# Performance work log

Measured on AMD Instinct MI355X. Metric: run time of the kernel, lower is better.

The kernel has to match this reference:

```python
import jax, jax.numpy as jnp
import numpy as np

T = 0.07          # temperature (params[1])
B, N, D, C = 128, 100000, 128, 40  # batch, bank size (outputSize=K), feat dim (inputSize-1), n classes
STDV = 1.0 / np.sqrt((D + 1) / 3.0)  # init scale from __init__


def setup_inputs() -> dict:
    key = jax.random.key(0)
    k1, k2, k3, k4, k5, k6 = jax.random.split(key, 6)
    x = jax.random.normal(k1, (B, D), dtype=jnp.float32)
    x = x / jnp.linalg.norm(x, axis=1, keepdims=True)  # unit-norm features (keeps exp(out/T) in range)
    y = jax.random.randint(k2, (B,), 0, N)
    labels = jax.random.randint(k3, (B,), 0, C)
    bank_labels = jax.random.randint(k4, (N,), 0, C).astype(jnp.float32)
    mem_feats = (jax.random.uniform(k5, (N, D), dtype=jnp.float32) * 2.0 - 1.0) * STDV
    da_feats = (jax.random.uniform(k6, (N, D), dtype=jnp.float32) * 2.0 - 1.0) * STDV
    memory = jnp.concatenate([bank_labels[:, None], mem_feats], axis=1)      # [N, 1+D], col 0 = label
    memory_da = jnp.concatenate([bank_labels[:, None], da_feats], axis=1)    # [N, 1+D], col 0 = label
    return {"x": x, "y": y, "labels": labels, "memory_da": memory_da, "memory": memory}


def reference(x, y, labels, memory_da, memory):
    # NCEFunction.forward: out[b,n] = exp(x[b] . memory_da[n,1:] / T), Z-normalized per row (Z<0 branch)
    n_out = memory_da.shape[0]
    feats = memory_da[:, 1:]                               # [N, D] gathered features
    out = jnp.exp(jnp.einsum('bd,nd->bn', x, feats) / T)   # [B, N] (torch bmm over repeated bank)
    Z1 = out.mean(axis=1, keepdims=True) * n_out           # per-row Z estimate
    out = out / Z1
    # idx: per-label torch.where loop -> expressed densely as a boolean match matrix [B, N]
    idx_mask = memory_da[None, :, 0] == labels[:, None].astype(memory_da.dtype)
    return out, idx_mask
```

## Files before the change

### kernel.cpp

```cpp
#include <hip/hip_runtime.h>
#include <hip/hip_bf16.h>

#define NB 128
#define NMEM 100000
#define ND 128
constexpr float T_INV = 1.0f / 0.07f;

constexpr int LROW = ND + 8;
constexpr int TILE = 128;
constexpr int NTILES = (NMEM + TILE - 1) / TILE;
constexpr int ZSTRIDE = 16;

typedef __attribute__((ext_vector_type(8))) __bf16 bf16x8;
typedef __attribute__((ext_vector_type(4))) float f32x4;

template<bool PASS2>
__global__ __launch_bounds__(256, 2) void nce_pass(
    const float* __restrict__ x,
    const int* __restrict__ labels,
    const float* __restrict__ mem_da,
    float* __restrict__ zbuf,
    float* __restrict__ out,
    float* __restrict__ maskout)
{
  __shared__ __bf16 xs[NB * LROW];
  __shared__ __bf16 fs[TILE * LROW];
  __shared__ float lbl_n[TILE];
  __shared__ float lbl_b[NB];
  __shared__ float rz[NB];
  __shared__ float zl[NB];

  const int tid = threadIdx.x;
  const int t = blockIdx.x;

  const float4* x4 = (const float4*)x;
  #pragma unroll
  for (int i = 0; i < 16; ++i) {
    int g4 = tid + i * 256;
    float4 v = x4[g4];
    int row = g4 >> 5;
    int col = (g4 & 31) * 4;
    __bf16* p = &xs[row * LROW + col];
    p[0] = (__bf16)v.x; p[1] = (__bf16)v.y; p[2] = (__bf16)v.z; p[3] = (__bf16)v.w;
  }

  const int rows = min(TILE, NMEM - t * TILE);
  const int count4 = rows * 129 / 4;
  const float4* f4 = (const float4*)(mem_da + (size_t)t * (TILE * 129));
  for (int i = tid; i < count4; i += 256) {
    float4 v = f4[i];
    unsigned g = 4u * (unsigned)i;
    #pragma unroll
    for (int c = 0; c < 4; ++c) {
      float val = (&v.x)[c];
      unsigned gg = g + c;
      unsigned r = gg / 129u;
      unsigned cc = gg - r * 129u;
      if (cc == 0) lbl_n[r] = val;
      else fs[r * LROW + (cc - 1)] = (__bf16)val;
    }
  }

  if (PASS2) {
    if (tid < NB) {
      lbl_b[tid] = (float)labels[tid];
      rz[tid] = 1.0f / zbuf[tid * ZSTRIDE];
    }
  } else {
    if (tid < NB) zl[tid] = 0.0f;
  }
  __syncthreads();

  const int wid = tid >> 6;
  const int lane = tid & 63;
  const int q = lane >> 4;
  const int l16 = lane & 15;
  const int nbase = t * TILE + wid * 32;

  if (nbase < NMEM) {
    f32x4 acc[8][2];
    #pragma unroll
    for (int mt = 0; mt < 8; ++mt) {
      acc[mt][0] = (f32x4){0.f, 0.f, 0.f, 0.f};
      acc[mt][1] = (f32x4){0.f, 0.f, 0.f, 0.f};
    }

    #pragma unroll
    for (int kc = 0; kc < 4; ++kc) {
      const int ko = kc * 32 + q * 8;
      bf16x8 b0 = *(const bf16x8*)&fs[(wid * 32 + l16) * LROW + ko];
      bf16x8 b1 = *(const bf16x8*)&fs[(wid * 32 + 16 + l16) * LROW + ko];
      #pragma unroll
      for (int mt = 0; mt < 8; ++mt) {
        bf16x8 a = *(const bf16x8*)&xs[(mt * 16 + l16) * LROW + ko];
        acc[mt][0] = __builtin_amdgcn_mfma_f32_16x16x32_bf16(a, b0, acc[mt][0], 0, 0, 0);
        acc[mt][1] = __builtin_amdgcn_mfma_f32_16x16x32_bf16(a, b1, acc[mt][1], 0, 0, 0);
      }
    }

    if (!PASS2) {
      #pragma unroll
      for (int mt = 0; mt < 8; ++mt) {
        #pragma unroll
        for (int r = 0; r < 4; ++r) {
          float v = __expf(acc[mt][0][r] * T_INV) + __expf(acc[mt][1][r] * T_INV);
          v += __shfl_xor(v, 1);
          v += __shfl_xor(v, 2);
          v += __shfl_xor(v, 4);
          v += __shfl_xor(v, 8);
          if (l16 == 0) atomicAdd(&zl[mt * 16 + q * 4 + r], v);
        }
      }
    } else {
      float ln0 = lbl_n[wid * 32 + l16];
      float ln1 = lbl_n[wid * 32 + 16 + l16];
      #pragma unroll
      for (int mt = 0; mt < 8; ++mt) {
        #pragma unroll
        for (int r = 0; r < 4; ++r) {
          int m = mt * 16 + q * 4 + r;
          float rzm = rz[m];
          float lb = lbl_b[m];
          size_t base = (size_t)m * NMEM + nbase + l16;
          out[base]      = __expf(acc[mt][0][r] * T_INV) * rzm;
          out[base + 16] = __expf(acc[mt][1][r] * T_INV) * rzm;
          maskout[base]      = (ln0 == lb) ? 1.0f : 0.0f;
          maskout[base + 16] = (ln1 == lb) ? 1.0f : 0.0f;
        }
      }
    }
  }

  if (!PASS2) {
    __syncthreads();
    if (tid < NB) atomicAdd(&zbuf[tid * ZSTRIDE], zl[tid]);
  }
}

extern "C" void kernel_launch(void* const* d_in, const int* in_sizes, int n_in,
                              void* d_out, int out_size, void* d_ws, size_t ws_size,
                              hipStream_t stream) {
  const float* x      = (const float*)d_in[0];
  const int* labels   = (const int*)d_in[2];
  const float* mem_da = (const float*)d_in[3];
  float* out     = (float*)d_out;
  float* maskout = out + (size_t)NB * NMEM;
  float* zbuf    = (float*)d_ws;

  hipMemsetAsync(zbuf, 0, NB * ZSTRIDE * sizeof(float), stream);
  nce_pass<false><<<NTILES, 256, 0, stream>>>(x, labels, mem_da, zbuf, nullptr, nullptr);
  nce_pass<true ><<<NTILES, 256, 0, stream>>>(x, labels, mem_da, zbuf, out, maskout);
}
```

Before: 237.1 us.

## Move mask writes into pass 1 and batch global loads into registers

Moves the label-match mask stores from the second pass into the first, which previously only computed the Z sums. This splits the output write traffic evenly across the two kernels so pass 1's idle write bandwidth is used. It also issues all memory-bank and x loads into registers up front before converting them into shared memory, to keep more loads in flight, and replaces the per-element divide by 129 with an incremental counter. Holding these values in registers raises register pressure, which may hurt occupancy under the 256x2 launch bounds.

Measured after the change: 224.9 us. 5.1% less time.

```diff
diff --git a/kernel.cpp b/kernel.cpp
--- a/kernel.cpp
+++ b/kernel.cpp
@@ -10,9 +10,12 @@
 constexpr int TILE = 128;
 constexpr int NTILES = (NMEM + TILE - 1) / TILE;
 constexpr int ZSTRIDE = 16;
+constexpr int C4FULL = TILE * 129 / 4;
+constexpr int NITER = (C4FULL + 255) / 256;
 
 typedef __attribute__((ext_vector_type(8))) __bf16 bf16x8;
 typedef __attribute__((ext_vector_type(4))) float f32x4;
+struct bf4 { __bf16 a, b, c, d; };
 
 template<bool PASS2>
 __global__ __launch_bounds__(256, 2) void nce_pass(
@@ -32,42 +35,51 @@
 
   const int tid = threadIdx.x;
   const int t = blockIdx.x;
+  const int count4 = (t == NTILES - 1) ? (NMEM - t * TILE) * 129 / 4 : C4FULL;
 
+  const float4* f4 = (const float4*)(mem_da + (size_t)t * (TILE * 129));
+  float4 fv[NITER];
+  #pragma unroll
+  for (int i = 0; i < NITER; ++i) {
+    int idx = tid + i * 256;
+    fv[i] = f4[idx < count4 ? idx : 0];
+  }
   const float4* x4 = (const float4*)x;
+  float4 xv[16];
+  #pragma unroll
+  for (int i = 0; i < 16; ++i) xv[i] = x4[tid + i * 256];
+
   #pragma unroll
   for (int i = 0; i < 16; ++i) {
     int g4 = tid + i * 256;
-    float4 v = x4[g4];
     int row = g4 >> 5;
     int col = (g4 & 31) * 4;
-    __bf16* p = &xs[row * LROW + col];
-    p[0] = (__bf16)v.x; p[1] = (__bf16)v.y; p[2] = (__bf16)v.z; p[3] = (__bf16)v.w;
+    *(bf4*)&xs[row * LROW + col] =
+        bf4{(__bf16)xv[i].x, (__bf16)xv[i].y, (__bf16)xv[i].z, (__bf16)xv[i].w};
   }
 
-  const int rows = min(TILE, NMEM - t * TILE);
-  const int count4 = rows * 129 / 4;
-  const float4* f4 = (const float4*)(mem_da + (size_t)t * (TILE * 129));
-  for (int i = tid; i < count4; i += 256) {
-    float4 v = f4[i];
-    unsigned g = 4u * (unsigned)i;
-    #pragma unroll
-    for (int c = 0; c < 4; ++c) {
-      float val = (&v.x)[c];
-      unsigned gg = g + c;
-      unsigned r = gg / 129u;
-      unsigned cc = gg - r * 129u;
-      if (cc == 0) lbl_n[r] = val;
-      else fs[r * LROW + (cc - 1)] = (__bf16)val;
+  #pragma unroll
+  for (int i = 0; i < NITER; ++i) {
+    int idx = tid + i * 256;
+    if (idx < count4) {
+      unsigned g = 4u * (unsigned)idx;
+      unsigned r = g / 129u;
+      unsigned cc = g - r * 129u;
+      float4 v = fv[i];
+      #pragma unroll
+      for (int c = 0; c < 4; ++c) {
+        float val = (&v.x)[c];
+        if (cc == 0) lbl_n[r] = val;
+        else fs[r * LROW + (cc - 1)] = (__bf16)val;
+        if (++cc == 129u) { cc = 0; ++r; }
+      }
     }
   }
 
-  if (PASS2) {
-    if (tid < NB) {
-      lbl_b[tid] = (float)labels[tid];
-      rz[tid] = 1.0f / zbuf[tid * ZSTRIDE];
-    }
-  } else {
-    if (tid < NB) zl[tid] = 0.0f;
+  if (tid < NB) {
+    lbl_b[tid] = (float)labels[tid];
+    if (PASS2) rz[tid] = 1.0f / zbuf[tid * ZSTRIDE];
+    else zl[tid] = 0.0f;
   }
   __syncthreads();
 
@@ -84,7 +96,6 @@
       acc[mt][0] = (f32x4){0.f, 0.f, 0.f, 0.f};
       acc[mt][1] = (f32x4){0.f, 0.f, 0.f, 0.f};
     }
-
     #pragma unroll
     for (int kc = 0; kc < 4; ++kc) {
       const int ko = kc * 32 + q * 8;
@@ -99,19 +110,6 @@
     }
 
     if (!PASS2) {
-      #pragma unroll
-      for (int mt = 0; mt < 8; ++mt) {
-        #pragma unroll
-        for (int r = 0; r < 4; ++r) {
-          float v = __expf(acc[mt][0][r] * T_INV) + __expf(acc[mt][1][r] * T_INV);
-          v += __shfl_xor(v, 1);
-          v += __shfl_xor(v, 2);
-          v += __shfl_xor(v, 4);
-          v += __shfl_xor(v, 8);
-          if (l16 == 0) atomicAdd(&zl[mt * 16 + q * 4 + r], v);
-        }
-      }
-    } else {
       float ln0 = lbl_n[wid * 32 + l16];
       float ln1 = lbl_n[wid * 32 + 16 + l16];
       #pragma unroll
@@ -119,13 +117,28 @@
         #pragma unroll
         for (int r = 0; r < 4; ++r) {
           int m = mt * 16 + q * 4 + r;
+          float lb = lbl_b[m];
+          size_t base = (size_t)m * NMEM + nbase + l16;
+          maskout[base]      = (ln0 == lb) ? 1.0f : 0.0f;
+          maskout[base + 16] = (ln1 == lb) ? 1.0f : 0.0f;
+          float v = __expf(acc[mt][0][r] * T_INV) + __expf(acc[mt][1][r] * T_INV);
+          v += __shfl_xor(v, 1);
+          v += __shfl_xor(v, 2);
+          v += __shfl_xor(v, 4);
+          v += __shfl_xor(v, 8);
+          if (l16 == 0) atomicAdd(&zl[m], v);
+        }
+      }
+    } else {
+      #pragma unroll
+      for (int mt = 0; mt < 8; ++mt) {
+        #pragma unroll
+        for (int r = 0; r < 4; ++r) {
+          int m = mt * 16 + q * 4 + r;
           float rzm = rz[m];
-          float lb = lbl_b[m];
           size_t base = (size_t)m * NMEM + nbase + l16;
           out[base]      = __expf(acc[mt][0][r] * T_INV) * rzm;
           out[base + 16] = __expf(acc[mt][1][r] * T_INV) * rzm;
-          maskout[base]      = (ln0 == lb) ? 1.0f : 0.0f;
-          maskout[base + 16] = (ln1 == lb) ? 1.0f : 0.0f;
         }
       }
     }
@@ -148,6 +161,6 @@
   float* zbuf    = (float*)d_ws;
 
   hipMemsetAsync(zbuf, 0, NB * ZSTRIDE * sizeof(float), stream);
-  nce_pass<false><<<NTILES, 256, 0, stream>>>(x, labels, mem_da, zbuf, nullptr, nullptr);
-  nce_pass<true ><<<NTILES, 256, 0, stream>>>(x, labels, mem_da, zbuf, out, maskout);
+  nce_pass<false><<<NTILES, 256, 0, stream>>>(x, labels, mem_da, zbuf, nullptr, maskout);
+  nce_pass<true ><<<NTILES, 256, 0, stream>>>(x, labels, mem_da, zbuf, out, nullptr);
 }
```

## Use persistent per-wave loops, load bank rows directly to registers, split mask write

Applied to the files above, without the earlier changes.

Replaces the one-block-per-128-row-tile grid with a persistent grid of 512 blocks. Each wave loops over 16-row bank chunks and loads the bf16 B operand straight from global memory into registers, with no LDS staging. The x tile is staged in LDS once per block, and Z partial sums are kept in registers until a single reduction at the end, which cuts the per-tile shuffle and atomic traffic. The mask write moves into pass 1 so the two passes split the output store traffic more evenly. The risk is that the per-lane strided 32-byte loads of 129-float rows coalesce poorly.

Result: faster. 207.7 us (-12.4%).

```diff
diff --git a/kernel.cpp b/kernel.cpp
--- a/kernel.cpp
+++ b/kernel.cpp
@@ -7,15 +7,17 @@
 constexpr float T_INV = 1.0f / 0.07f;
 
 constexpr int LROW = ND + 8;
-constexpr int TILE = 128;
-constexpr int NTILES = (NMEM + TILE - 1) / TILE;
+constexpr int NTW = NMEM / 16;
+constexpr int GRID = 512;
+constexpr int NWAVES = GRID * 4;
 constexpr int ZSTRIDE = 16;
 
 typedef __attribute__((ext_vector_type(8))) __bf16 bf16x8;
 typedef __attribute__((ext_vector_type(4))) float f32x4;
+struct bf4 { __bf16 a, b, c, d; };
 
 template<bool PASS2>
-__global__ __launch_bounds__(256, 2) void nce_pass(
+__global__ __launch_bounds__(256, 2) void nce_wave(
     const float* __restrict__ x,
     const int* __restrict__ labels,
     const float* __restrict__ mem_da,
@@ -24,114 +26,94 @@
     float* __restrict__ maskout)
 {
   __shared__ __bf16 xs[NB * LROW];
-  __shared__ __bf16 fs[TILE * LROW];
-  __shared__ float lbl_n[TILE];
-  __shared__ float lbl_b[NB];
-  __shared__ float rz[NB];
+  __shared__ float aux[NB];
   __shared__ float zl[NB];
 
   const int tid = threadIdx.x;
-  const int t = blockIdx.x;
 
   const float4* x4 = (const float4*)x;
+  float4 xv[16];
+  #pragma unroll
+  for (int i = 0; i < 16; ++i) xv[i] = x4[tid + i * 256];
   #pragma unroll
   for (int i = 0; i < 16; ++i) {
     int g4 = tid + i * 256;
-    float4 v = x4[g4];
-    int row = g4 >> 5;
-    int col = (g4 & 31) * 4;
-    __bf16* p = &xs[row * LROW + col];
-    p[0] = (__bf16)v.x; p[1] = (__bf16)v.y; p[2] = (__bf16)v.z; p[3] = (__bf16)v.w;
+    *(bf4*)&xs[(g4 >> 5) * LROW + (g4 & 31) * 4] =
+        bf4{(__bf16)xv[i].x, (__bf16)xv[i].y, (__bf16)xv[i].z, (__bf16)xv[i].w};
   }
-
-  const int rows = min(TILE, NMEM - t * TILE);
-  const int count4 = rows * 129 / 4;
-  const float4* f4 = (const float4*)(mem_da + (size_t)t * (TILE * 129));
-  for (int i = tid; i < count4; i += 256) {
-    float4 v = f4[i];
-    unsigned g = 4u * (unsigned)i;
-    #pragma unroll
-    for (int c = 0; c < 4; ++c) {
-      float val = (&v.x)[c];
-      unsigned gg = g + c;
-      unsigned r = gg / 129u;
-      unsigned cc = gg - r * 129u;
-      if (cc == 0) lbl_n[r] = val;
-      else fs[r * LROW + (cc - 1)] = (__bf16)val;
-    }
-  }
-
-  if (PASS2) {
-    if (tid < NB) {
-      lbl_b[tid] = (float)labels[tid];
-      rz[tid] = 1.0f / zbuf[tid * ZSTRIDE];
-    }
-  } else {
-    if (tid < NB) zl[tid] = 0.0f;
+  if (tid < NB) {
+    if (PASS2) aux[tid] = 1.0f / zbuf[tid * ZSTRIDE];
+    else { aux[tid] = (float)labels[tid]; zl[tid] = 0.f; }
   }
   __syncthreads();
 
-  const int wid = tid >> 6;
-  const int lane = tid & 63;
-  const int q = lane >> 4;
-  const int l16 = lane & 15;
-  const int nbase = t * TILE + wid * 32;
+  const int wid = tid >> 6, lane = tid & 63, q = lane >> 4, l16 = lane & 15;
+  const int wgid = blockIdx.x * 4 + wid;
 
-  if (nbase < NMEM) {
-    f32x4 acc[8][2];
+  f32x4 am[8];
+  #pragma unroll
+  for (int mt = 0; mt < 8; ++mt) am[mt] = *(const f32x4*)&aux[mt * 16 + q * 4];
+
+  f32x4 zacc[8];
+  #pragma unroll
+  for (int mt = 0; mt < 8; ++mt) zacc[mt] = (f32x4){0.f, 0.f, 0.f, 0.f};
+
+  for (int t = wgid; t < NTW; t += NWAVES) {
+    const float* rowp = mem_da + (size_t)(t * 16 + l16) * 129;
+    float ln;
+    if (!PASS2) ln = rowp[0];
+    float bf[4][8];
     #pragma unroll
-    for (int mt = 0; mt < 8; ++mt) {
-      acc[mt][0] = (f32x4){0.f, 0.f, 0.f, 0.f};
-      acc[mt][1] = (f32x4){0.f, 0.f, 0.f, 0.f};
-    }
+    for (int kc = 0; kc < 4; ++kc)
+      __builtin_memcpy(&bf[kc][0], rowp + 1 + kc * 32 + q * 8, 32);
+    bf16x8 bb[4];
+    #pragma unroll
+    for (int kc = 0; kc < 4; ++kc)
+      #pragma unroll
+      for (int j = 0; j < 8; ++j) bb[kc][j] = (__bf16)bf[kc][j];
 
+    f32x4 acc[8];
+    #pragma unroll
+    for (int mt = 0; mt < 8; ++mt) acc[mt] = (f32x4){0.f, 0.f, 0.f, 0.f};
     #pragma unroll
     for (int kc = 0; kc < 4; ++kc) {
       const int ko = kc * 32 + q * 8;
-      bf16x8 b0 = *(const bf16x8*)&fs[(wid * 32 + l16) * LROW + ko];
-      bf16x8 b1 = *(const bf16x8*)&fs[(wid * 32 + 16 + l16) * LROW + ko];
       #pragma unroll
       for (int mt = 0; mt < 8; ++mt) {
         bf16x8 a = *(const bf16x8*)&xs[(mt * 16 + l16) * LROW + ko];
-        acc[mt][0] = __builtin_amdgcn_mfma_f32_16x16x32_bf16(a, b0, acc[mt][0], 0, 0, 0);
-        acc[mt][1] = __builtin_amdgcn_mfma_f32_16x16x32_bf16(a, b1, acc[mt][1], 0, 0, 0);
+        acc[mt] = __builtin_amdgcn_mfma_f32_16x16x32_bf16(a, bb[kc], acc[mt], 0, 0, 0);
       }
     }
 
-    if (!PASS2) {
+    const size_t n = (size_t)t * 16 + l16;
+    #pragma unroll
+    for (int mt = 0; mt < 8; ++mt) {
       #pragma unroll
-      for (int mt = 0; mt < 8; ++mt) {
-        #pragma unroll
-        for (int r = 0; r < 4; ++r) {
-          float v = __expf(acc[mt][0][r] * T_INV) + __expf(acc[mt][1][r] * T_INV);
-          v += __shfl_xor(v, 1);
-          v += __shfl_xor(v, 2);
-          v += __shfl_xor(v, 4);
-          v += __shfl_xor(v, 8);
-          if (l16 == 0) atomicAdd(&zl[mt * 16 + q * 4 + r], v);
-        }
-      }
-    } else {
-      float ln0 = lbl_n[wid * 32 + l16];
-      float ln1 = lbl_n[wid * 32 + 16 + l16];
-      #pragma unroll
-      for (int mt = 0; mt < 8; ++mt) {
-        #pragma unroll
-        for (int r = 0; r < 4; ++r) {
-          int m = mt * 16 + q * 4 + r;
-          float rzm = rz[m];
-          float lb = lbl_b[m];
-          size_t base = (size_t)m * NMEM + nbase + l16;
-          out[base]      = __expf(acc[mt][0][r] * T_INV) * rzm;
-          out[base + 16] = __expf(acc[mt][1][r] * T_INV) * rzm;
-          maskout[base]      = (ln0 == lb) ? 1.0f : 0.0f;
-          maskout[base + 16] = (ln1 == lb) ? 1.0f : 0.0f;
+      for (int r = 0; r < 4; ++r) {
+        const size_t off = (size_t)(mt * 16 + q * 4 + r) * NMEM + n;
+        if (!PASS2) {
+          zacc[mt][r] += __expf(acc[mt][r] * T_INV);
+          maskout[off] = (ln == am[mt][r]) ? 1.0f : 0.0f;
+        } else {
+          out[off] = __expf(acc[mt][r] * T_INV) * am[mt][r];
         }
       }
     }
   }
 
   if (!PASS2) {
+    #pragma unroll
+    for (int mt = 0; mt < 8; ++mt) {
+      #pragma unroll
+      for (int r = 0; r < 4; ++r) {
+        float v = zacc[mt][r];
+        v += __shfl_xor(v, 1);
+        v += __shfl_xor(v, 2);
+        v += __shfl_xor(v, 4);
+        v += __shfl_xor(v, 8);
+        if (l16 == 0) atomicAdd(&zl[mt * 16 + q * 4 + r], v);
+      }
+    }
     __syncthreads();
     if (tid < NB) atomicAdd(&zbuf[tid * ZSTRIDE], zl[tid]);
   }
@@ -148,6 +130,6 @@
   float* zbuf    = (float*)d_ws;
 
   hipMemsetAsync(zbuf, 0, NB * ZSTRIDE * sizeof(float), stream);
-  nce_pass<false><<<NTILES, 256, 0, stream>>>(x, labels, mem_da, zbuf, nullptr, nullptr);
-  nce_pass<true ><<<NTILES, 256, 0, stream>>>(x, labels, mem_da, zbuf, out, maskout);
+  nce_wave<false><<<GRID, 256, 0, stream>>>(x, labels, mem_da, zbuf, nullptr, maskout);
+  nce_wave<true ><<<GRID, 256, 0, stream>>>(x, labels, mem_da, zbuf, out, nullptr);
 }
```
